# Performance work log

Hardware: AMD Instinct MI355X
Metric: run time of the kernel (lower is better)

The kernel has to match this reference:

```python
import jax, jax.numpy as jnp
import numpy as np
from jax import lax

NEG = -1e9
B, H, C, TX, TY = 4, 256, 80, 256, 1024  # batch, hidden, mel bins, text len, mel len


def setup_inputs() -> dict:
    key = jax.random.key(0)
    k = jax.random.split(key, 6)
    en = jax.random.normal(k[0], (B, H, TX), jnp.float32)
    mu = jax.random.normal(k[1], (B, C, TX), jnp.float32)
    log_sigma = 0.1 * jax.random.normal(k[2], (B, C, TX), jnp.float32)
    y = jax.random.normal(k[3], (B, C, TY), jnp.float32)
    x_lengths = jax.random.randint(k[4], (B,), TX // 2, TX + 1, jnp.int32)
    y_lengths = jax.random.randint(k[5], (B,), TY // 2, TY + 1, jnp.int32)
    return {"en": en, "mu": mu, "log_sigma": log_sigma, "y": y,
            "x_lengths": x_lengths, "y_lengths": y_lengths}


def sequence_mask(lengths, max_len):
    return jnp.arange(max_len)[None, :] < lengths[:, None]


def compute_log_probs(mu, log_sigma, y):
    # y: [B,C,Ty] -> [B,1,Ty,C]; mu/log_sigma: [B,C,Tx] -> [B,Tx,1,C]
    yb = jnp.transpose(y, (0, 2, 1))[:, None]
    mub = jnp.transpose(mu, (0, 2, 1))[:, :, None]
    lsb = jnp.transpose(log_sigma, (0, 2, 1))[:, :, None]
    # mse / sigma^2 = (y-mu)^2 * exp(-2*log_sigma); mean over channel dim
    expo = -0.5 * jnp.mean((yb - mub) ** 2 * jnp.exp(-2.0 * lsb), axis=-1)  # [B,Tx,Ty]
    return expo - 0.5 * jnp.mean(lsb, axis=-1)  # broadcast [B,Tx,1] -> [B,Tx,Ty]


def maximum_path(logp, mask, x_lengths, y_lengths):
    """Monotonic alignment search (Glow-TTS Viterbi DP), vectorized over batch."""
    b, tx, ty = logp.shape
    lp = jnp.where(mask > 0, logp, NEG)
    cols = jnp.moveaxis(lp, 2, 0)  # [Ty, B, Tx]
    v0 = jnp.broadcast_to(jnp.where(jnp.arange(tx) == 0, 0.0, NEG), (b, tx)).astype(logp.dtype)

    def fwd(v, col):
        v_shift = jnp.concatenate([jnp.full((b, 1), NEG, v.dtype), v[:, :-1]], axis=1)
        diag = v_shift > v  # come from (x-1, y-1) rather than (x, y-1)
        return col + jnp.maximum(v, v_shift), diag

    _, diags = lax.scan(fwd, v0, cols)  # diags: [Ty, B, Tx] bool

    xs_idx = jnp.arange(tx)

    def bwd(idx, inp):
        yv, dcol = inp
        active = yv < y_lengths  # [B]
        row = (xs_idx[None, :] == idx[:, None]) & active[:, None]
        d = jnp.take_along_axis(dcol, idx[:, None], axis=1)[:, 0]
        idx = jnp.where(active & (idx > 0) & d, idx - 1, idx)
        return idx, row

    _, rows = lax.scan(bwd, x_lengths - 1, (jnp.arange(ty), diags), reverse=True)
    return lax.stop_gradient(jnp.moveaxis(rows, 0, 2).astype(logp.dtype))  # [B,Tx,Ty]


def generate_path(dr, mask):
    # dr: [B,Tx] durations; mask: [B,Tx,Ty]
    ty = mask.shape[-1]
    cum = jnp.cumsum(dr, axis=1)
    pm = (jnp.arange(ty)[None, None, :] < cum[:, :, None]).astype(dr.dtype)
    path = pm - jnp.pad(pm, ((0, 0), (1, 0), (0, 0)))[:, :-1]
    return path * mask


def reference(en, mu, log_sigma, y, x_lengths, y_lengths):
    tx, ty = mu.shape[-1], y.shape[-1]
    x_mask = sequence_mask(x_lengths, tx).astype(jnp.float32)  # [B,Tx]
    y_mask = sequence_mask(y_lengths, ty).astype(jnp.float32)  # [B,Ty]
    attn_mask = x_mask[:, :, None] * y_mask[:, None, :]        # [B,Tx,Ty]
    logp = compute_log_probs(mu, log_sigma, y)
    attn = maximum_path(logp, attn_mask, x_lengths, y_lengths)
    dr_mas = jnp.sum(attn, axis=-1)                            # durations [B,Tx]
    path = generate_path(dr_mas, attn_mask)                    # convert_dr_to_align
    # expand_encoder_outputs: attn^T @ en^T -> [B,H,Ty]
    o_en_ex = jnp.einsum('bxy,bhx->bhy', path, en)
    return o_en_ex, logp, attn, dr_mas
```

## Files before the change

### kernel.cpp

```cpp
#include <hip/hip_runtime.h>
#include <cstdint>
#include <cmath>

#define B_ 4
#define H_ 256
#define C_ 80
#define TX_ 256
#define TY_ 1024
#define NEGF (-1e9f)

#define OFF_LOGP (B_*H_*TY_)
#define OFF_ATTN (OFF_LOGP + B_*TX_*TY_)
#define OFF_DR   (OFF_ATTN + B_*TX_*TY_)

__device__ __forceinline__ float dpp_shr1_negfill_f32(float x) {
  union { float f; int i; } u, o, r;
  u.f = x; o.f = NEGF;
  r.i = __builtin_amdgcn_update_dpp(o.i, u.i, 0x138, 0xf, 0xf, false);
  return r.f;
}

__global__ __launch_bounds__(256) void k_logp(
    const float* __restrict__ mu, const float* __restrict__ ls,
    const float* __restrict__ y, const int* __restrict__ xlp,
    const int* __restrict__ ylp, float* __restrict__ logp_out,
    float* __restrict__ lpT)
{
  const int b  = blockIdx.y;
  const int x0 = blockIdx.x * 4;
  const int tid = threadIdx.x;
  __shared__ double s_w[4][C_];
  __shared__ double s_m1[4][C_];
  __shared__ double s_wm2[4][C_];
  __shared__ double s_lsv[4][C_];
  __shared__ double s_K[4];
  __shared__ double s_t0[4];
  __shared__ float tile[TY_][4];
  for (int i = tid; i < 4 * C_; i += 256) {
    int xi = i / C_, c = i - xi * C_;
    double m = (double)mu[(b * C_ + c) * TX_ + x0 + xi];
    double l = (double)ls[(b * C_ + c) * TX_ + x0 + xi];
    double w = exp(-2.0 * l);
    s_w[xi][c]   = w;
    s_m1[xi][c]  = -2.0 * w * m;
    s_wm2[xi][c] = w * m * m;
    s_lsv[xi][c] = l;
  }
  __syncthreads();
  {
    int xi = tid >> 6, cc = tid & 63;
    double kp = (cc < C_) ? s_wm2[xi][cc] : 0.0;
    double tp = (cc < C_) ? s_lsv[xi][cc] : 0.0;
    if (cc + 64 < C_) { kp += s_wm2[xi][cc + 64]; tp += s_lsv[xi][cc + 64]; }
#pragma unroll
    for (int off = 32; off; off >>= 1) {
      kp += __shfl_down(kp, off);
      tp += __shfl_down(tp, off);
    }
    if (cc == 0) { s_K[xi] = kp; s_t0[xi] = -0.5 * (tp * (1.0 / C_)); }
  }
  __syncthreads();

  const int t0 = tid * 4;
  double acc[4][4];
#pragma unroll
  for (int xi = 0; xi < 4; ++xi)
#pragma unroll
    for (int k = 0; k < 4; ++k) acc[xi][k] = 0.0;

  const float4* yp = (const float4*)(y + (size_t)b * C_ * TY_) + tid;
#pragma unroll 4
  for (int c = 0; c < C_; ++c) {
    float4 yv = yp[c * (TY_ / 4)];
    double y0 = yv.x, y1 = yv.y, y2 = yv.z, y3 = yv.w;
#pragma unroll
    for (int xi = 0; xi < 4; ++xi) {
      double w = s_w[xi][c], m1 = s_m1[xi][c];
      double u0 = fma(w, y0, m1), u1 = fma(w, y1, m1);
      double u2 = fma(w, y2, m1), u3 = fma(w, y3, m1);
      acc[xi][0] = fma(u0, y0, acc[xi][0]);
      acc[xi][1] = fma(u1, y1, acc[xi][1]);
      acc[xi][2] = fma(u2, y2, acc[xi][2]);
      acc[xi][3] = fma(u3, y3, acc[xi][3]);
    }
  }

  const int xlen = xlp[b], ylen = ylp[b];
#pragma unroll
  for (int xi = 0; xi < 4; ++xi) {
    int x = x0 + xi;
    double c0 = s_t0[xi], K = s_K[xi];
    float r[4];
#pragma unroll
    for (int k = 0; k < 4; ++k)
      r[k] = (float)((acc[xi][k] + K) * (-0.5 / C_) + c0);
    *(float4*)&logp_out[((size_t)(b * TX_ + x)) * TY_ + t0] =
        make_float4(r[0], r[1], r[2], r[3]);
    bool xm = x < xlen;
#pragma unroll
    for (int k = 0; k < 4; ++k)
      tile[t0 + k][xi] = (xm && (t0 + k) < ylen) ? r[k] : NEGF;
  }
  __syncthreads();

  float* dst = lpT + (size_t)b * TY_ * TX_ + x0;
  const float4* tp = (const float4*)tile;
#pragma unroll
  for (int k = 0; k < 4; ++k) {
    int t = tid + 256 * k;
    *(float4*)&dst[(size_t)t * TX_] = tp[t];
  }
}

#define POLL_FLAG(i)                                                     \
  { while (vflag[i] == 0u) __builtin_amdgcn_s_sleep(1);                  \
    asm volatile("" ::: "memory"); }

#define DP_CHUNK(SHBASE)                                                 \
  _Pragma("unroll")                                                      \
  for (int u = 0; u < 16; ++u) {                                         \
    float4 col = rr[u & 7];                                              \
    rr[u & 7] = (u < 8) ? pA[(u + 8) * 64 + lane]                        \
                        : pB[(u - 8) * 64 + lane];                       \
    float sh = dpp_shr1_negfill_f32(v3);                                 \
    float m0 = fmaxf(v0, sh);                                            \
    float m1 = fmaxf(v1, v0);                                            \
    float m2 = fmaxf(v2, v1);                                            \
    float m3 = fmaxf(v3, v2);                                            \
    w0 |= (__float_as_uint(v0 - m0) >> 31) << ((SHBASE) + u);            \
    w1 |= (__float_as_uint(v1 - m1) >> 31) << ((SHBASE) + u);            \
    w2 |= (__float_as_uint(v2 - m2) >> 31) << ((SHBASE) + u);            \
    w3 |= (__float_as_uint(v3 - m3) >> 31) << ((SHBASE) + u);            \
    v0 = col.x + m0;                                                     \
    v1 = col.y + m1;                                                     \
    v2 = col.z + m2;                                                     \
    v3 = col.w + m3;                                                     \
  }

__global__ __launch_bounds__(256, 1) void k_dp(
    const float* __restrict__ lpT, const int* __restrict__ xlp,
    const int* __restrict__ ylp, float* __restrict__ dr_out,
    int* __restrict__ cum_ws, int* __restrict__ xt_ws)
{
  const int b = blockIdx.x;
  const int tid = threadIdx.x;
  const int lane = tid & 63;
  const int w = tid >> 6;
  __shared__ __align__(16) float    ring[6 * 16 * 256];
  __shared__ __align__(16) uint32_t bits[8192];
  __shared__ __align__(16) uint32_t dur[TX_];
  __shared__ uint32_t flags[64];
  __shared__ int      prog;

  const float4* gb4   = (const float4*)(lpT + (size_t)b * TY_ * TX_);
  const float4* ring4 = (const float4*)ring;

  const int ylen = ylp[b];
  const int nch  = ((ylen + 31) >> 5) << 1;

  if (tid < 64) flags[tid] = 0u;
  if (tid == 0) prog = -1;
  __syncthreads();

  if (w == 0) {
    volatile uint32_t* vflag = flags;
    volatile int*      vprog = &prog;
    POLL_FLAG(0);
    float4 rr[8];
#pragma unroll
    for (int i = 0; i < 8; ++i) rr[i] = ring4[i * 64 + lane];

    float v0 = (lane == 0) ? 0.0f : NEGF;
    float v1 = NEGF, v2 = NEGF, v3 = NEGF;
    uint32_t w0 = 0, w1 = 0, w2 = 0, w3 = 0;
    int sA = 0, sB = 1;
    const float4* pA;
    const float4* pB;

    for (int cp = 0; cp < nch; cp += 2) {
      { int nf = (cp + 1 < nch) ? cp + 1 : nch - 1; POLL_FLAG(nf); }
      pA = ring4 + sA * 1024; pB = ring4 + sB * 1024;
      DP_CHUNK(0)
      asm volatile("" ::: "memory");
      *vprog = cp;
      sA = sB; sB = (sB == 5) ? 0 : sB + 1;

      { int nf = (cp + 2 < nch) ? cp + 2 : nch - 1; POLL_FLAG(nf); }
      pA = ring4 + sA * 1024; pB = ring4 + sB * 1024;
      DP_CHUNK(16)
      *(uint4*)&bits[(cp >> 1) * 256 + 4 * lane] = make_uint4(w0, w1, w2, w3);
      w0 = w1 = w2 = w3 = 0;
      asm volatile("" ::: "memory");
      *vprog = cp + 1;
      sA = sB; sB = (sB == 5) ? 0 : sB + 1;
    }
  } else {
    const int p = w - 1;
    volatile int*      vprog = &prog;
    volatile uint32_t* vflag = flags;
    for (int c = p; c < nch; c += 3) {
      const int need = c - 6;
      while (*vprog < need) __builtin_amdgcn_s_sleep(8);
      asm volatile("" ::: "memory");
      const float4* src = gb4 + (size_t)(c * 16) * 64 + lane;
      float4 tmp[16];
#pragma unroll
      for (int r = 0; r < 16; ++r) tmp[r] = src[r * 64];
      float4* dst = (float4*)&ring[(c % 6) * 4096] + lane;
#pragma unroll
      for (int r = 0; r < 16; ++r) dst[r * 64] = tmp[r];
      asm volatile("s_waitcnt lgkmcnt(0)" ::: "memory");
      vflag[c] = 1u;
    }
  }

  __syncthreads();
  dur[tid] = 0;
  __syncthreads();

  const int xlen = xlp[b];
  if (tid == 0) {
    int idx = xlen - 1;
    int t = ylen - 1;
    while (t >= 0) {
      if (idx == 0) { dur[0] = (uint32_t)(t + 1); break; }
      int ww = t >> 5, rrm = t & 31;
      uint32_t wd = bits[ww * 256 + idx];
      wd &= (rrm == 31) ? 0xffffffffu : ((1u << (rrm + 1)) - 1u);
      while (wd == 0 && ww > 0) { --ww; wd = bits[ww * 256 + idx]; }
      if (wd == 0) { dur[idx] = (uint32_t)(t + 1); break; }
      int bitpos = 31 - __builtin_clz(wd);
      int tp = (ww << 5) | bitpos;
      dur[idx] = (uint32_t)(t - tp + 1);
      --idx;
      t = tp - 1;
    }
  }
  __syncthreads();

  if (w == 0) {
    uint32_t d0 = dur[4 * lane], d1 = dur[4 * lane + 1];
    uint32_t d2 = dur[4 * lane + 2], d3 = dur[4 * lane + 3];
    uint32_t own = d0 + d1 + d2 + d3;
    uint32_t s = own;
#pragma unroll
    for (int off = 1; off < 64; off <<= 1) {
      uint32_t n = __shfl_up(s, off);
      if (lane >= off) s += n;
    }
    uint32_t base = s - own;
    uint32_t c0 = base + d0, c1 = c0 + d1, c2 = c1 + d2, c3 = c2 + d3;
    int x = 4 * lane;
    cum_ws[b * TX_ + x]     = (int)c0;
    cum_ws[b * TX_ + x + 1] = (int)c1;
    cum_ws[b * TX_ + x + 2] = (int)c2;
    cum_ws[b * TX_ + x + 3] = (int)c3;
    dr_out[b * TX_ + x]     = (float)d0;
    dr_out[b * TX_ + x + 1] = (float)d1;
    dr_out[b * TX_ + x + 2] = (float)d2;
    dr_out[b * TX_ + x + 3] = (float)d3;
    int* xt = xt_ws + b * TY_;
    for (uint32_t t = c0 - d0; t < c0; ++t) xt[t] = x;
    for (uint32_t t = c1 - d1; t < c1; ++t) xt[t] = x + 1;
    for (uint32_t t = c2 - d2; t < c2; ++t) xt[t] = x + 2;
    for (uint32_t t = c3 - d3; t < c3; ++t) xt[t] = x + 3;
  }
}

__global__ __launch_bounds__(256) void k_epi(
    const int* __restrict__ cum_ws, const int* __restrict__ xt_ws,
    const float* __restrict__ en, const int* __restrict__ ylp,
    float* __restrict__ attn, float* __restrict__ oen)
{
  const int b = blockIdx.y, bx = blockIdx.x, tid = threadIdx.x;
  __shared__ float row[TX_];
  if (bx < TX_) {
    const int x = bx;
    int hi = cum_ws[b * TX_ + x];
    int lo = (x > 0) ? cum_ws[b * TX_ + x - 1] : 0;
    int t0 = tid * 4;
    float4 v;
    v.x = (t0     >= lo && t0     < hi) ? 1.f : 0.f;
    v.y = (t0 + 1 >= lo && t0 + 1 < hi) ? 1.f : 0.f;
    v.z = (t0 + 2 >= lo && t0 + 2 < hi) ? 1.f : 0.f;
    v.w = (t0 + 3 >= lo && t0 + 3 < hi) ? 1.f : 0.f;
    *(float4*)&attn[((size_t)(b * TX_ + x)) * TY_ + t0] = v;
  } else {
    const int h = bx - TX_;
    row[tid] = en[((size_t)(b * H_ + h)) * TX_ + tid];
    __syncthreads();
    const int ylen = ylp[b];
    int t0 = tid * 4;
    int4 xi = *(const int4*)&xt_ws[b * TY_ + t0];
    float4 v;
    v.x = (t0     < ylen) ? row[xi.x & (TX_ - 1)] : 0.f;
    v.y = (t0 + 1 < ylen) ? row[xi.y & (TX_ - 1)] : 0.f;
    v.z = (t0 + 2 < ylen) ? row[xi.z & (TX_ - 1)] : 0.f;
    v.w = (t0 + 3 < ylen) ? row[xi.w & (TX_ - 1)] : 0.f;
    *(float4*)&oen[((size_t)(b * H_ + h)) * TY_ + t0] = v;
  }
}

extern "C" void kernel_launch(void* const* d_in, const int* in_sizes, int n_in,
                              void* d_out, int out_size, void* d_ws, size_t ws_size,
                              hipStream_t stream)
{
  const float* en = (const float*)d_in[0];
  const float* mu = (const float*)d_in[1];
  const float* ls = (const float*)d_in[2];
  const float* y  = (const float*)d_in[3];
  const int*   xl = (const int*)d_in[4];
  const int*   yl = (const int*)d_in[5];

  float* out  = (float*)d_out;
  float* oen  = out;
  float* logp = out + OFF_LOGP;
  float* attn = out + OFF_ATTN;
  float* dr   = out + OFF_DR;

  int* cum = (int*)d_ws;
  int* xt  = cum + B_ * TX_;

  k_logp<<<dim3(TX_ / 4, B_),   256, 0, stream>>>(mu, ls, y, xl, yl, logp, attn);
  k_dp  <<<B_,                  256, 0, stream>>>(attn, xl, yl, dr, cum, xt);
  k_epi <<<dim3(TX_ + H_, B_),  256, 0, stream>>>(cum, xt, en, yl, attn, oen);
}
```

Before: 180.0 us.

## Fuse logp, DP and epilogue kernels into one persistent kernel with global flags

Merges the three kernels (logp, Viterbi DP, expansion epilogue) into a single 256-block launch. Blocks signal per-batch completion through device-scope atomic counters and spin-wait on them instead of relying on kernel boundaries. This removes two launch gaps and lets the epilogue start per batch as soon as that batch's DP is done. It adds a memset launch, depends on all 256 blocks being co-resident (1 block/CU with 96KB+ LDS), and makes every block carry the large shared-memory footprint.

```diff
diff --git a/kernel.cpp b/kernel.cpp
--- a/kernel.cpp
+++ b/kernel.cpp
@@ -18,98 +18,6 @@
   u.f = x; o.f = NEGF;
   r.i = __builtin_amdgcn_update_dpp(o.i, u.i, 0x138, 0xf, 0xf, false);
   return r.f;
-}
-
-__global__ __launch_bounds__(256) void k_logp(
-    const float* __restrict__ mu, const float* __restrict__ ls,
-    const float* __restrict__ y, const int* __restrict__ xlp,
-    const int* __restrict__ ylp, float* __restrict__ logp_out,
-    float* __restrict__ lpT)
-{
-  const int b  = blockIdx.y;
-  const int x0 = blockIdx.x * 4;
-  const int tid = threadIdx.x;
-  __shared__ double s_w[4][C_];
-  __shared__ double s_m1[4][C_];
-  __shared__ double s_wm2[4][C_];
-  __shared__ double s_lsv[4][C_];
-  __shared__ double s_K[4];
-  __shared__ double s_t0[4];
-  __shared__ float tile[TY_][4];
-  for (int i = tid; i < 4 * C_; i += 256) {
-    int xi = i / C_, c = i - xi * C_;
-    double m = (double)mu[(b * C_ + c) * TX_ + x0 + xi];
-    double l = (double)ls[(b * C_ + c) * TX_ + x0 + xi];
-    double w = exp(-2.0 * l);
-    s_w[xi][c]   = w;
-    s_m1[xi][c]  = -2.0 * w * m;
-    s_wm2[xi][c] = w * m * m;
-    s_lsv[xi][c] = l;
-  }
-  __syncthreads();
-  {
-    int xi = tid >> 6, cc = tid & 63;
-    double kp = (cc < C_) ? s_wm2[xi][cc] : 0.0;
-    double tp = (cc < C_) ? s_lsv[xi][cc] : 0.0;
-    if (cc + 64 < C_) { kp += s_wm2[xi][cc + 64]; tp += s_lsv[xi][cc + 64]; }
-#pragma unroll
-    for (int off = 32; off; off >>= 1) {
-      kp += __shfl_down(kp, off);
-      tp += __shfl_down(tp, off);
-    }
-    if (cc == 0) { s_K[xi] = kp; s_t0[xi] = -0.5 * (tp * (1.0 / C_)); }
-  }
-  __syncthreads();
-
-  const int t0 = tid * 4;
-  double acc[4][4];
-#pragma unroll
-  for (int xi = 0; xi < 4; ++xi)
-#pragma unroll
-    for (int k = 0; k < 4; ++k) acc[xi][k] = 0.0;
-
-  const float4* yp = (const float4*)(y + (size_t)b * C_ * TY_) + tid;
-#pragma unroll 4
-  for (int c = 0; c < C_; ++c) {
-    float4 yv = yp[c * (TY_ / 4)];
-    double y0 = yv.x, y1 = yv.y, y2 = yv.z, y3 = yv.w;
-#pragma unroll
-    for (int xi = 0; xi < 4; ++xi) {
-      double w = s_w[xi][c], m1 = s_m1[xi][c];
-      double u0 = fma(w, y0, m1), u1 = fma(w, y1, m1);
-      double u2 = fma(w, y2, m1), u3 = fma(w, y3, m1);
-      acc[xi][0] = fma(u0, y0, acc[xi][0]);
-      acc[xi][1] = fma(u1, y1, acc[xi][1]);
-      acc[xi][2] = fma(u2, y2, acc[xi][2]);
-      acc[xi][3] = fma(u3, y3, acc[xi][3]);
-    }
-  }
-
-  const int xlen = xlp[b], ylen = ylp[b];
-#pragma unroll
-  for (int xi = 0; xi < 4; ++xi) {
-    int x = x0 + xi;
-    double c0 = s_t0[xi], K = s_K[xi];
-    float r[4];
-#pragma unroll
-    for (int k = 0; k < 4; ++k)
-      r[k] = (float)((acc[xi][k] + K) * (-0.5 / C_) + c0);
-    *(float4*)&logp_out[((size_t)(b * TX_ + x)) * TY_ + t0] =
-        make_float4(r[0], r[1], r[2], r[3]);
-    bool xm = x < xlen;
-#pragma unroll
-    for (int k = 0; k < 4; ++k)
-      tile[t0 + k][xi] = (xm && (t0 + k) < ylen) ? r[k] : NEGF;
-  }
-  __syncthreads();
-
-  float* dst = lpT + (size_t)b * TY_ * TX_ + x0;
-  const float4* tp = (const float4*)tile;
-#pragma unroll
-  for (int k = 0; k < 4; ++k) {
-    int t = tid + 256 * k;
-    *(float4*)&dst[(size_t)t * TX_] = tp[t];
-  }
 }
 
 #define POLL_FLAG(i)                                                     \
@@ -137,167 +45,290 @@
     v3 = col.w + m3;                                                     \
   }
 
-__global__ __launch_bounds__(256, 1) void k_dp(
-    const float* __restrict__ lpT, const int* __restrict__ xlp,
-    const int* __restrict__ ylp, float* __restrict__ dr_out,
-    int* __restrict__ cum_ws, int* __restrict__ xt_ws)
+__global__ __launch_bounds__(256, 1) void k_fused(
+    const float* __restrict__ en, const float* __restrict__ mu,
+    const float* __restrict__ ls, const float* __restrict__ y,
+    const int* __restrict__ xlp, const int* __restrict__ ylp,
+    float* __restrict__ oen, float* __restrict__ logp_out,
+    float* __restrict__ attn,
+    float* __restrict__ dr_out,
+    int* __restrict__ cum_ws, int* __restrict__ xt_ws,
+    int* __restrict__ gflags)
 {
-  const int b = blockIdx.x;
+  const int bid = blockIdx.x;
   const int tid = threadIdx.x;
-  const int lane = tid & 63;
-  const int w = tid >> 6;
-  __shared__ __align__(16) float    ring[6 * 16 * 256];
+
+  __shared__ __align__(16) char     arena[96 * 1024];
   __shared__ __align__(16) uint32_t bits[8192];
   __shared__ __align__(16) uint32_t dur[TX_];
-  __shared__ uint32_t flags[64];
-  __shared__ int      prog;
-
-  const float4* gb4   = (const float4*)(lpT + (size_t)b * TY_ * TX_);
-  const float4* ring4 = (const float4*)ring;
-
-  const int ylen = ylp[b];
-  const int nch  = ((ylen + 31) >> 5) << 1;
-
-  if (tid < 64) flags[tid] = 0u;
-  if (tid == 0) prog = -1;
+  __shared__ uint32_t dflags[64];
+  __shared__ int      dprog;
+
+  float* lpT = attn;
+
+  {
+    const int b  = bid >> 6;
+    const int x0 = (bid & 63) * 4;
+    double (*s_w)[C_]   = (double(*)[C_])(arena);
+    double (*s_m1)[C_]  = (double(*)[C_])(arena + 2560);
+    double (*s_wm2)[C_] = (double(*)[C_])(arena + 5120);
+    double (*s_lsv)[C_] = (double(*)[C_])(arena + 7680);
+    double* s_K  = (double*)(arena + 10240);
+    double* s_t0 = (double*)(arena + 10272);
+    float (*tile)[4] = (float(*)[4])(arena + 10304);
+
+    for (int i = tid; i < 4 * C_; i += 256) {
+      int xi = i / C_, c = i - xi * C_;
+      double m = (double)mu[(b * C_ + c) * TX_ + x0 + xi];
+      double l = (double)ls[(b * C_ + c) * TX_ + x0 + xi];
+      double w = exp(-2.0 * l);
+      s_w[xi][c]   = w;
+      s_m1[xi][c]  = -2.0 * w * m;
+      s_wm2[xi][c] = w * m * m;
+      s_lsv[xi][c] = l;
+    }
+    __syncthreads();
+    {
+      int xi = tid >> 6, cc = tid & 63;
+      double kp = (cc < C_) ? s_wm2[xi][cc] : 0.0;
+      double tp = (cc < C_) ? s_lsv[xi][cc] : 0.0;
+      if (cc + 64 < C_) { kp += s_wm2[xi][cc + 64]; tp += s_lsv[xi][cc + 64]; }
+#pragma unroll
+      for (int off = 32; off; off >>= 1) {
+        kp += __shfl_down(kp, off);
+        tp += __shfl_down(tp, off);
+      }
+      if (cc == 0) { s_K[xi] = kp; s_t0[xi] = -0.5 * (tp * (1.0 / C_)); }
+    }
+    __syncthreads();
+
+    const int t0 = tid * 4;
+    double acc[4][4];
+#pragma unroll
+    for (int xi = 0; xi < 4; ++xi)
+#pragma unroll
+      for (int k = 0; k < 4; ++k) acc[xi][k] = 0.0;
+
+    const float4* yp = (const float4*)(y + (size_t)b * C_ * TY_) + tid;
+#pragma unroll 4
+    for (int c = 0; c < C_; ++c) {
+      float4 yv = yp[c * (TY_ / 4)];
+      double y0 = yv.x, y1 = yv.y, y2 = yv.z, y3 = yv.w;
+#pragma unroll
+      for (int xi = 0; xi < 4; ++xi) {
+        double w = s_w[xi][c], m1 = s_m1[xi][c];
+        double u0 = fma(w, y0, m1), u1 = fma(w, y1, m1);
+        double u2 = fma(w, y2, m1), u3 = fma(w, y3, m1);
+        acc[xi][0] = fma(u0, y0, acc[xi][0]);
+        acc[xi][1] = fma(u1, y1, acc[xi][1]);
+        acc[xi][2] = fma(u2, y2, acc[xi][2]);
+        acc[xi][3] = fma(u3, y3, acc[xi][3]);
+      }
+    }
+
+    const int xlen = xlp[b], ylen = ylp[b];
+#pragma unroll
+    for (int xi = 0; xi < 4; ++xi) {
+      int x = x0 + xi;
+      double c0 = s_t0[xi], K = s_K[xi];
+      float r[4];
+#pragma unroll
+      for (int k = 0; k < 4; ++k)
+        r[k] = (float)((acc[xi][k] + K) * (-0.5 / C_) + c0);
+      *(float4*)&logp_out[((size_t)(b * TX_ + x)) * TY_ + t0] =
+          make_float4(r[0], r[1], r[2], r[3]);
+      bool xm = x < xlen;
+#pragma unroll
+      for (int k = 0; k < 4; ++k)
+        tile[t0 + k][xi] = (xm && (t0 + k) < ylen) ? r[k] : NEGF;
+    }
+    __syncthreads();
+
+    float* dst = lpT + (size_t)b * TY_ * TX_ + x0;
+    const float4* tp = (const float4*)tile;
+#pragma unroll
+    for (int k = 0; k < 4; ++k) {
+      int t = tid + 256 * k;
+      *(float4*)&dst[(size_t)t * TX_] = tp[t];
+    }
+  }
+  __threadfence();
   __syncthreads();
-
-  if (w == 0) {
-    volatile uint32_t* vflag = flags;
-    volatile int*      vprog = &prog;
-    POLL_FLAG(0);
-    float4 rr[8];
-#pragma unroll
-    for (int i = 0; i < 8; ++i) rr[i] = ring4[i * 64 + lane];
-
-    float v0 = (lane == 0) ? 0.0f : NEGF;
-    float v1 = NEGF, v2 = NEGF, v3 = NEGF;
-    uint32_t w0 = 0, w1 = 0, w2 = 0, w3 = 0;
-    int sA = 0, sB = 1;
-    const float4* pA;
-    const float4* pB;
-
-    for (int cp = 0; cp < nch; cp += 2) {
-      { int nf = (cp + 1 < nch) ? cp + 1 : nch - 1; POLL_FLAG(nf); }
-      pA = ring4 + sA * 1024; pB = ring4 + sB * 1024;
-      DP_CHUNK(0)
-      asm volatile("" ::: "memory");
-      *vprog = cp;
-      sA = sB; sB = (sB == 5) ? 0 : sB + 1;
-
-      { int nf = (cp + 2 < nch) ? cp + 2 : nch - 1; POLL_FLAG(nf); }
-      pA = ring4 + sA * 1024; pB = ring4 + sB * 1024;
-      DP_CHUNK(16)
-      *(uint4*)&bits[(cp >> 1) * 256 + 4 * lane] = make_uint4(w0, w1, w2, w3);
-      w0 = w1 = w2 = w3 = 0;
-      asm volatile("" ::: "memory");
-      *vprog = cp + 1;
-      sA = sB; sB = (sB == 5) ? 0 : sB + 1;
-    }
-  } else {
-    const int p = w - 1;
-    volatile int*      vprog = &prog;
-    volatile uint32_t* vflag = flags;
-    for (int c = p; c < nch; c += 3) {
-      const int need = c - 6;
-      while (*vprog < need) __builtin_amdgcn_s_sleep(8);
-      asm volatile("" ::: "memory");
-      const float4* src = gb4 + (size_t)(c * 16) * 64 + lane;
-      float4 tmp[16];
-#pragma unroll
-      for (int r = 0; r < 16; ++r) tmp[r] = src[r * 64];
-      float4* dst = (float4*)&ring[(c % 6) * 4096] + lane;
-#pragma unroll
-      for (int r = 0; r < 16; ++r) dst[r * 64] = tmp[r];
-      asm volatile("s_waitcnt lgkmcnt(0)" ::: "memory");
-      vflag[c] = 1u;
-    }
+  if (tid == 0)
+    __hip_atomic_fetch_add(&gflags[bid >> 6], 1, __ATOMIC_RELEASE,
+                           __HIP_MEMORY_SCOPE_AGENT);
+
+  if (bid < B_) {
+    const int b = bid;
+    if (tid == 0) {
+      while (__hip_atomic_load(&gflags[b], __ATOMIC_ACQUIRE,
+                               __HIP_MEMORY_SCOPE_AGENT) < 64)
+        __builtin_amdgcn_s_sleep(8);
+    }
+    __syncthreads();
+
+    const int lane = tid & 63;
+    const int w = tid >> 6;
+    float* ring = (float*)arena;
+    const float4* gb4   = (const float4*)(lpT + (size_t)b * TY_ * TX_);
+    const float4* ring4 = (const float4*)ring;
+
+    const int ylen = ylp[b];
+    const int nch  = ((ylen + 31) >> 5) << 1;
+
+    if (tid < 64) dflags[tid] = 0u;
+    if (tid == 0) dprog = -1;
+    __syncthreads();
+
+    if (w == 0) {
+      volatile uint32_t* vflag = dflags;
+      volatile int*      vprog = &dprog;
+      POLL_FLAG(0);
+      float4 rr[8];
+#pragma unroll
+      for (int i = 0; i < 8; ++i) rr[i] = ring4[i * 64 + lane];
+
+      float v0 = (lane == 0) ? 0.0f : NEGF;
+      float v1 = NEGF, v2 = NEGF, v3 = NEGF;
+      uint32_t w0 = 0, w1 = 0, w2 = 0, w3 = 0;
+      int sA = 0, sB = 1;
+      const float4* pA;
+      const float4* pB;
+
+      for (int cp = 0; cp < nch; cp += 2) {
+        { int nf = (cp + 1 < nch) ? cp + 1 : nch - 1; POLL_FLAG(nf); }
+        pA = ring4 + sA * 1024; pB = ring4 + sB * 1024;
+        DP_CHUNK(0)
+        asm volatile("" ::: "memory");
+        *vprog = cp;
+        sA = sB; sB = (sB == 5) ? 0 : sB + 1;
+
+        { int nf = (cp + 2 < nch) ? cp + 2 : nch - 1; POLL_FLAG(nf); }
+        pA = ring4 + sA * 1024; pB = ring4 + sB * 1024;
+        DP_CHUNK(16)
+        *(uint4*)&bits[(cp >> 1) * 256 + 4 * lane] = make_uint4(w0, w1, w2, w3);
+        w0 = w1 = w2 = w3 = 0;
+        asm volatile("" ::: "memory");
+        *vprog = cp + 1;
+        sA = sB; sB = (sB == 5) ? 0 : sB + 1;
+      }
+    } else {
+      const int p = w - 1;
+      volatile int*      vprog = &dprog;
+      volatile uint32_t* vflag = dflags;
+      for (int c = p; c < nch; c += 3) {
+        const int need = c - 6;
+        while (*vprog < need) __builtin_amdgcn_s_sleep(8);
+        asm volatile("" ::: "memory");
+        const float4* src = gb4 + (size_t)(c * 16) * 64 + lane;
+        float4 tmp[16];
+#pragma unroll
+        for (int r = 0; r < 16; ++r) tmp[r] = src[r * 64];
+        float4* dst = (float4*)&ring[(c % 6) * 4096] + lane;
+#pragma unroll
+        for (int r = 0; r < 16; ++r) dst[r * 64] = tmp[r];
+        asm volatile("s_waitcnt lgkmcnt(0)" ::: "memory");
+        vflag[c] = 1u;
+      }
+    }
+
+    __syncthreads();
+    dur[tid] = 0;
+    __syncthreads();
+
+    const int xlen = xlp[b];
+    if (tid == 0) {
+      int idx = xlen - 1;
+      int t = ylen - 1;
+      while (t >= 0) {
+        if (idx == 0) { dur[0] = (uint32_t)(t + 1); break; }
+        int ww = t >> 5, rrm = t & 31;
+        uint32_t wd = bits[ww * 256 + idx];
+        wd &= (rrm == 31) ? 0xffffffffu : ((1u << (rrm + 1)) - 1u);
+        while (wd == 0 && ww > 0) { --ww; wd = bits[ww * 256 + idx]; }
+        if (wd == 0) { dur[idx] = (uint32_t)(t + 1); break; }
+        int bitpos = 31 - __builtin_clz(wd);
+        int tp = (ww << 5) | bitpos;
+        dur[idx] = (uint32_t)(t - tp + 1);
+        --idx;
+        t = tp - 1;
+      }
+    }
+    __syncthreads();
+
+    if (w == 0) {
+      uint32_t d0 = dur[4 * lane], d1 = dur[4 * lane + 1];
+      uint32_t d2 = dur[4 * lane + 2], d3 = dur[4 * lane + 3];
+      uint32_t own = d0 + d1 + d2 + d3;
+      uint32_t s = own;
+#pragma unroll
+      for (int off = 1; off < 64; off <<= 1) {
+        uint32_t n = __shfl_up(s, off);
+        if (lane >= off) s += n;
+      }
+      uint32_t base = s - own;
+      uint32_t c0 = base + d0, c1 = c0 + d1, c2 = c1 + d2, c3 = c2 + d3;
+      int x = 4 * lane;
+      cum_ws[b * TX_ + x]     = (int)c0;
+      cum_ws[b * TX_ + x + 1] = (int)c1;
+      cum_ws[b * TX_ + x + 2] = (int)c2;
+      cum_ws[b * TX_ + x + 3] = (int)c3;
+      dr_out[b * TX_ + x]     = (float)d0;
+      dr_out[b * TX_ + x + 1] = (float)d1;
+      dr_out[b * TX_ + x + 2] = (float)d2;
+      dr_out[b * TX_ + x + 3] = (float)d3;
+      int* xt = xt_ws + b * TY_;
+      for (uint32_t t = c0 - d0; t < c0; ++t) xt[t] = x;
+      for (uint32_t t = c1 - d1; t < c1; ++t) xt[t] = x + 1;
+      for (uint32_t t = c2 - d2; t < c2; ++t) xt[t] = x + 2;
+      for (uint32_t t = c3 - d3; t < c3; ++t) xt[t] = x + 3;
+    }
+    __threadfence();
+    __syncthreads();
+    if (tid == 0)
+      __hip_atomic_store(&gflags[B_ + b], 1, __ATOMIC_RELEASE,
+                         __HIP_MEMORY_SCOPE_AGENT);
   }
 
-  __syncthreads();
-  dur[tid] = 0;
-  __syncthreads();
-
-  const int xlen = xlp[b];
-  if (tid == 0) {
-    int idx = xlen - 1;
-    int t = ylen - 1;
-    while (t >= 0) {
-      if (idx == 0) { dur[0] = (uint32_t)(t + 1); break; }
-      int ww = t >> 5, rrm = t & 31;
-      uint32_t wd = bits[ww * 256 + idx];
-      wd &= (rrm == 31) ? 0xffffffffu : ((1u << (rrm + 1)) - 1u);
-      while (wd == 0 && ww > 0) { --ww; wd = bits[ww * 256 + idx]; }
-      if (wd == 0) { dur[idx] = (uint32_t)(t + 1); break; }
-      int bitpos = 31 - __builtin_clz(wd);
-      int tp = (ww << 5) | bitpos;
-      dur[idx] = (uint32_t)(t - tp + 1);
-      --idx;
-      t = tp - 1;
-    }
-  }
-  __syncthreads();
-
-  if (w == 0) {
-    uint32_t d0 = dur[4 * lane], d1 = dur[4 * lane + 1];
-    uint32_t d2 = dur[4 * lane + 2], d3 = dur[4 * lane + 3];
-    uint32_t own = d0 + d1 + d2 + d3;
-    uint32_t s = own;
-#pragma unroll
-    for (int off = 1; off < 64; off <<= 1) {
-      uint32_t n = __shfl_up(s, off);
-      if (lane >= off) s += n;
-    }
-    uint32_t base = s - own;
-    uint32_t c0 = base + d0, c1 = c0 + d1, c2 = c1 + d2, c3 = c2 + d3;
-    int x = 4 * lane;
-    cum_ws[b * TX_ + x]     = (int)c0;
-    cum_ws[b * TX_ + x + 1] = (int)c1;
-    cum_ws[b * TX_ + x + 2] = (int)c2;
-    cum_ws[b * TX_ + x + 3] = (int)c3;
-    dr_out[b * TX_ + x]     = (float)d0;
-    dr_out[b * TX_ + x + 1] = (float)d1;
-    dr_out[b * TX_ + x + 2] = (float)d2;
-    dr_out[b * TX_ + x + 3] = (float)d3;
-    int* xt = xt_ws + b * TY_;
-    for (uint32_t t = c0 - d0; t < c0; ++t) xt[t] = x;
-    for (uint32_t t = c1 - d1; t < c1; ++t) xt[t] = x + 1;
-    for (uint32_t t = c2 - d2; t < c2; ++t) xt[t] = x + 2;
-    for (uint32_t t = c3 - d3; t < c3; ++t) xt[t] = x + 3;
-  }
-}
-
-__global__ __launch_bounds__(256) void k_epi(
-    const int* __restrict__ cum_ws, const int* __restrict__ xt_ws,
-    const float* __restrict__ en, const int* __restrict__ ylp,
-    float* __restrict__ attn, float* __restrict__ oen)
-{
-  const int b = blockIdx.y, bx = blockIdx.x, tid = threadIdx.x;
-  __shared__ float row[TX_];
-  if (bx < TX_) {
-    const int x = bx;
-    int hi = cum_ws[b * TX_ + x];
-    int lo = (x > 0) ? cum_ws[b * TX_ + x - 1] : 0;
-    int t0 = tid * 4;
-    float4 v;
-    v.x = (t0     >= lo && t0     < hi) ? 1.f : 0.f;
-    v.y = (t0 + 1 >= lo && t0 + 1 < hi) ? 1.f : 0.f;
-    v.z = (t0 + 2 >= lo && t0 + 2 < hi) ? 1.f : 0.f;
-    v.w = (t0 + 3 >= lo && t0 + 3 < hi) ? 1.f : 0.f;
-    *(float4*)&attn[((size_t)(b * TX_ + x)) * TY_ + t0] = v;
-  } else {
-    const int h = bx - TX_;
-    row[tid] = en[((size_t)(b * H_ + h)) * TX_ + tid];
-    __syncthreads();
-    const int ylen = ylp[b];
-    int t0 = tid * 4;
-    int4 xi = *(const int4*)&xt_ws[b * TY_ + t0];
-    float4 v;
-    v.x = (t0     < ylen) ? row[xi.x & (TX_ - 1)] : 0.f;
-    v.y = (t0 + 1 < ylen) ? row[xi.y & (TX_ - 1)] : 0.f;
-    v.z = (t0 + 2 < ylen) ? row[xi.z & (TX_ - 1)] : 0.f;
-    v.w = (t0 + 3 < ylen) ? row[xi.w & (TX_ - 1)] : 0.f;
-    *(float4*)&oen[((size_t)(b * H_ + h)) * TY_ + t0] = v;
+  {
+    const int b3 = bid >> 6;
+    if (tid == 0) {
+      while (__hip_atomic_load(&gflags[B_ + b3], __ATOMIC_ACQUIRE,
+                               __HIP_MEMORY_SCOPE_AGENT) == 0)
+        __builtin_amdgcn_s_sleep(32);
+    }
+    __syncthreads();
+
+    float* row = (float*)dur;
+    const int ylen = ylp[b3];
+    const int t0 = tid * 4;
+#pragma unroll
+    for (int k = 0; k < 8; ++k) {
+      const int r = (bid & 63) * 8 + k;
+      if (r < TX_) {
+        const int x = r;
+        int hi = cum_ws[b3 * TX_ + x];
+        int lo = (x > 0) ? cum_ws[b3 * TX_ + x - 1] : 0;
+        float4 v;
+        v.x = (t0     >= lo && t0     < hi) ? 1.f : 0.f;
+        v.y = (t0 + 1 >= lo && t0 + 1 < hi) ? 1.f : 0.f;
+        v.z = (t0 + 2 >= lo && t0 + 2 < hi) ? 1.f : 0.f;
+        v.w = (t0 + 3 >= lo && t0 + 3 < hi) ? 1.f : 0.f;
+        *(float4*)&attn[((size_t)(b3 * TX_ + x)) * TY_ + t0] = v;
+      } else {
+        const int h = r - TX_;
+        __syncthreads();
+        row[tid] = en[((size_t)(b3 * H_ + h)) * TX_ + tid];
+        __syncthreads();
+        int4 xi = *(const int4*)&xt_ws[b3 * TY_ + t0];
+        float4 v;
+        v.x = (t0     < ylen) ? row[xi.x & (TX_ - 1)] : 0.f;
+        v.y = (t0 + 1 < ylen) ? row[xi.y & (TX_ - 1)] : 0.f;
+        v.z = (t0 + 2 < ylen) ? row[xi.z & (TX_ - 1)] : 0.f;
+        v.w = (t0 + 3 < ylen) ? row[xi.w & (TX_ - 1)] : 0.f;
+        *(float4*)&oen[((size_t)(b3 * H_ + h)) * TY_ + t0] = v;
+      }
+    }
   }
 }
 
@@ -318,10 +349,11 @@
   float* attn = out + OFF_ATTN;
   float* dr   = out + OFF_DR;
 
-  int* cum = (int*)d_ws;
-  int* xt  = cum + B_ * TX_;
-
-  k_logp<<<dim3(TX_ / 4, B_),   256, 0, stream>>>(mu, ls, y, xl, yl, logp, attn);
-  k_dp  <<<B_,                  256, 0, stream>>>(attn, xl, yl, dr, cum, xt);
-  k_epi <<<dim3(TX_ + H_, B_),  256, 0, stream>>>(cum, xt, en, yl, attn, oen);
+  int* cum    = (int*)d_ws;
+  int* xt     = cum + B_ * TX_;
+  int* gflags = xt + B_ * TY_;
+
+  hipMemsetAsync(gflags, 0, 8 * sizeof(int), stream);
+  k_fused<<<dim3(256), 256, 0, stream>>>(en, mu, ls, y, xl, yl,
+                                         oen, logp, attn, dr, cum, xt, gflags);
 }
```

New measurement: 232.5 us. 1.29x slower.

## Split logp kernel over Ty quarters so each thread handles one x row

Applied to the files above, without the earlier changes.

The log-prob kernel grid gains a third dimension that splits Ty into four 256-wide chunks. Each thread now accumulates four Ty points for a single x instead of four x rows, which cuts accumulator registers and gives four times as many blocks. The per-x weight and mean terms are packed into a double2 in shared memory. The cost is that the per-x setup (exp, reductions) is repeated in every Ty chunk, and each y element is read from global memory by more blocks.

```diff
diff --git a/kernel.cpp b/kernel.cpp
--- a/kernel.cpp
+++ b/kernel.cpp
@@ -26,29 +26,32 @@
     const int* __restrict__ ylp, float* __restrict__ logp_out,
     float* __restrict__ lpT)
 {
-  const int b  = blockIdx.y;
+  const int b  = blockIdx.z;
+  const int tq = blockIdx.y;
   const int x0 = blockIdx.x * 4;
   const int tid = threadIdx.x;
-  __shared__ double s_w[4][C_];
-  __shared__ double s_m1[4][C_];
-  __shared__ double s_wm2[4][C_];
-  __shared__ double s_lsv[4][C_];
-  __shared__ double s_K[4];
-  __shared__ double s_t0[4];
-  __shared__ float tile[TY_][4];
+  const int lane = tid & 63;
+  const int xi = tid >> 6;
+
+  __shared__ double2 s_wm[4][C_];
+  __shared__ double  s_wm2[4][C_];
+  __shared__ double  s_lsv[4][C_];
+  __shared__ double  s_K[4];
+  __shared__ double  s_t0[4];
+  __shared__ float   tile[256][4];
+
   for (int i = tid; i < 4 * C_; i += 256) {
-    int xi = i / C_, c = i - xi * C_;
-    double m = (double)mu[(b * C_ + c) * TX_ + x0 + xi];
-    double l = (double)ls[(b * C_ + c) * TX_ + x0 + xi];
+    int xj = i / C_, c = i - xj * C_;
+    double m = (double)mu[(b * C_ + c) * TX_ + x0 + xj];
+    double l = (double)ls[(b * C_ + c) * TX_ + x0 + xj];
     double w = exp(-2.0 * l);
-    s_w[xi][c]   = w;
-    s_m1[xi][c]  = -2.0 * w * m;
-    s_wm2[xi][c] = w * m * m;
-    s_lsv[xi][c] = l;
+    s_wm[xj][c]  = make_double2(w, -2.0 * w * m);
+    s_wm2[xj][c] = w * m * m;
+    s_lsv[xj][c] = l;
   }
   __syncthreads();
   {
-    int xi = tid >> 6, cc = tid & 63;
+    int cc = lane;
     double kp = (cc < C_) ? s_wm2[xi][cc] : 0.0;
     double tp = (cc < C_) ? s_lsv[xi][cc] : 0.0;
     if (cc + 64 < C_) { kp += s_wm2[xi][cc + 64]; tp += s_lsv[xi][cc + 64]; }
@@ -61,55 +64,46 @@
   }
   __syncthreads();
 
-  const int t0 = tid * 4;
-  double acc[4][4];
-#pragma unroll
-  for (int xi = 0; xi < 4; ++xi)
-#pragma unroll
-    for (int k = 0; k < 4; ++k) acc[xi][k] = 0.0;
-
-  const float4* yp = (const float4*)(y + (size_t)b * C_ * TY_) + tid;
+  double acc[4];
+#pragma unroll
+  for (int k = 0; k < 4; ++k) acc[k] = 0.0;
+
+  const float4* yp = (const float4*)(y + (size_t)b * C_ * TY_ + tq * 256) + lane;
 #pragma unroll 4
   for (int c = 0; c < C_; ++c) {
     float4 yv = yp[c * (TY_ / 4)];
     double y0 = yv.x, y1 = yv.y, y2 = yv.z, y3 = yv.w;
-#pragma unroll
-    for (int xi = 0; xi < 4; ++xi) {
-      double w = s_w[xi][c], m1 = s_m1[xi][c];
-      double u0 = fma(w, y0, m1), u1 = fma(w, y1, m1);
-      double u2 = fma(w, y2, m1), u3 = fma(w, y3, m1);
-      acc[xi][0] = fma(u0, y0, acc[xi][0]);
-      acc[xi][1] = fma(u1, y1, acc[xi][1]);
-      acc[xi][2] = fma(u2, y2, acc[xi][2]);
-      acc[xi][3] = fma(u3, y3, acc[xi][3]);
-    }
+    double2 wm = s_wm[xi][c];
+    double w = wm.x, m1 = wm.y;
+    double u0 = fma(w, y0, m1), u1 = fma(w, y1, m1);
+    double u2 = fma(w, y2, m1), u3 = fma(w, y3, m1);
+    acc[0] = fma(u0, y0, acc[0]);
+    acc[1] = fma(u1, y1, acc[1]);
+    acc[2] = fma(u2, y2, acc[2]);
+    acc[3] = fma(u3, y3, acc[3]);
   }
 
   const int xlen = xlp[b], ylen = ylp[b];
-#pragma unroll
-  for (int xi = 0; xi < 4; ++xi) {
-    int x = x0 + xi;
+  const int x  = x0 + xi;
+  const int t0 = tq * 256 + lane * 4;
+  {
     double c0 = s_t0[xi], K = s_K[xi];
     float r[4];
 #pragma unroll
     for (int k = 0; k < 4; ++k)
-      r[k] = (float)((acc[xi][k] + K) * (-0.5 / C_) + c0);
+      r[k] = (float)((acc[k] + K) * (-0.5 / C_) + c0);
     *(float4*)&logp_out[((size_t)(b * TX_ + x)) * TY_ + t0] =
         make_float4(r[0], r[1], r[2], r[3]);
     bool xm = x < xlen;
 #pragma unroll
     for (int k = 0; k < 4; ++k)
-      tile[t0 + k][xi] = (xm && (t0 + k) < ylen) ? r[k] : NEGF;
+      tile[lane * 4 + k][xi] = (xm && (t0 + k) < ylen) ? r[k] : NEGF;
   }
   __syncthreads();
 
   float* dst = lpT + (size_t)b * TY_ * TX_ + x0;
   const float4* tp = (const float4*)tile;
-#pragma unroll
-  for (int k = 0; k < 4; ++k) {
-    int t = tid + 256 * k;
-    *(float4*)&dst[(size_t)t * TX_] = tp[t];
-  }
+  *(float4*)&dst[(size_t)(tq * 256 + tid) * TX_] = tp[tid];
 }
 
 #define POLL_FLAG(i)                                                     \
@@ -321,7 +315,7 @@
   int* cum = (int*)d_ws;
   int* xt  = cum + B_ * TX_;
 
-  k_logp<<<dim3(TX_ / 4, B_),   256, 0, stream>>>(mu, ls, y, xl, yl, logp, attn);
-  k_dp  <<<B_,                  256, 0, stream>>>(attn, xl, yl, dr, cum, xt);
-  k_epi <<<dim3(TX_ + H_, B_),  256, 0, stream>>>(cum, xt, en, yl, attn, oen);
-}
+  k_logp<<<dim3(TX_ / 4, TY_ / 256, B_), 256, 0, stream>>>(mu, ls, y, xl, yl, logp, attn);
+  k_dp  <<<B_,                           256, 0, stream>>>(attn, xl, yl, dr, cum, xt);
+  k_epi <<<dim3(TX_ + H_, B_),           256, 0, stream>>>(cum, xt, en, yl, attn, oen);
+}
```

New measurement: 166.7 us. -7.4%, faster.
